# Kernel optimization log

Measured on AMD Instinct MI355X. Metric: run time of the kernel, lower is better.

Reference implementation:

```python
import math
import jax, jax.numpy as jnp
import numpy as np

B, N, D = 32, 1025, 768
K, CD, TD = 64, 128, 256  # num_clusters, cluster_dim, token_dim
REG = 0.1
NUM_ITERS = 5


def setup_inputs() -> dict:
    key = jax.random.key(0)
    ks = jax.random.split(key, 8)
    x = jax.random.normal(ks[0], (B, N, D), dtype=jnp.float32)
    # Linear params (torch nn.Linear: y = x @ W.T + b; we store W already transposed as [in, out])
    Wf = jax.random.normal(ks[1], (D, CD), dtype=jnp.float32) / math.sqrt(D)
    bf = jnp.zeros((CD,), dtype=jnp.float32)
    Ws = jax.random.normal(ks[2], (D, K), dtype=jnp.float32) / math.sqrt(D)
    bs = jnp.zeros((K,), dtype=jnp.float32)
    Wt = jax.random.normal(ks[3], (D, TD), dtype=jnp.float32) / math.sqrt(D)
    bt = jnp.zeros((TD,), dtype=jnp.float32)
    anchors = jax.random.normal(ks[4], (K, CD), dtype=jnp.float32) * 0.1
    dust_bin = jnp.float32(1.0)
    sharpness = jnp.float32(5.0)
    return {"x": x, "Wf": Wf, "bf": bf, "Ws": Ws, "bs": bs, "Wt": Wt, "bt": bt,
            "anchors": anchors, "dust_bin": dust_bin, "sharpness": sharpness}


def _log_otp_solver(log_a, log_b, M, num_iters, reg):
    M = M / reg
    u = jnp.zeros_like(log_a)  # [B, K+1]
    v = jnp.zeros_like(log_b)  # [B, N-1]
    for _ in range(num_iters):
        u = log_a - jax.nn.logsumexp(M + v[:, None, :], axis=2)
        v = log_b - jax.nn.logsumexp(M + u[:, :, None], axis=1)
    return M + u[:, :, None] + v[:, None, :]


def reference(x, Wf, bf, Ws, bs, Wt, bt, anchors, dust_bin, sharpness):
    b, n, d = x.shape
    t_global = x[:, 0]            # [B, D]
    fi = x[:, 1:]                 # [B, N-1, D]
    f = fi @ Wf + bf              # [B, N-1, CD]
    s = jnp.swapaxes(fi @ Ws + bs, 1, 2)  # [B, K, N-1]
    t = t_global @ Wt + bt        # [B, TD]
    s = s * sharpness
    dust = jnp.broadcast_to(dust_bin, (b, 1, n - 1))
    s_aug = jnp.concatenate([s, dust], axis=1)  # [B, K+1, N-1]
    log_a = jnp.full((b, K + 1), -math.log(K + 1), dtype=x.dtype)
    log_b = jnp.full((b, n - 1), -math.log(n - 1), dtype=x.dtype)
    log_P = _log_otp_solver(log_a, log_b, s_aug, NUM_ITERS, REG)
    p = jnp.exp(log_P)[:, :-1, :]  # [B, K, N-1]
    # v_agg = sum_n p[b,k,n] * (2*f[b,n,:] - anchors[k,:])  (algebraic rewrite of the broadcast sum)
    v_agg = 2.0 * jnp.einsum('bkn,bnc->bkc', p, f) - p.sum(axis=2)[:, :, None] * anchors[None]
    v_local = v_agg.reshape(b, -1)            # [B, K*CD]
    f_out = jnp.concatenate([t, v_local], axis=-1)
    norm = jnp.maximum(jnp.linalg.norm(f_out, axis=-1, keepdims=True), 1e-12)
    return f_out / norm
```

## Files before the change

### kernel.cpp

```cpp
#include <hip/hip_runtime.h>
#include <math.h>


#define BATCH 32
#define NTOK  1025
#define DIM   768
#define KDIM  64
#define CDIM  128
#define TDIM  256
#define NM1   1024
#define ROWLEN 8448
#define NITER 5
#define INV_REG 10.0f
#define NS_AGG 8
#define LOG_A (-4.17438727f)
#define LOG_B (-6.93147181f)

typedef __attribute__((ext_vector_type(8))) short short8;
typedef __attribute__((ext_vector_type(4))) float floatx4;

typedef __attribute__((address_space(3))) unsigned int lds_uint;
typedef const __attribute__((address_space(1))) unsigned int glb_uint;

__device__ __forceinline__ void gload_lds16(const void* g, void* l) {
    __builtin_amdgcn_global_load_lds((glb_uint*)g, (lds_uint*)l, 16, 0, 0);
}

__device__ __forceinline__ unsigned short bf16_rne(float f) {
    unsigned u = __builtin_bit_cast(unsigned, f);
    unsigned r = u + 0x7FFFu + ((u >> 16) & 1u);
    return (unsigned short)(r >> 16);
}

__device__ __forceinline__ short8 cvt8(float4 a, float4 b) {
    short8 r;
    r[0] = (short)bf16_rne(a.x); r[1] = (short)bf16_rne(a.y);
    r[2] = (short)bf16_rne(a.z); r[3] = (short)bf16_rne(a.w);
    r[4] = (short)bf16_rne(b.x); r[5] = (short)bf16_rne(b.y);
    r[6] = (short)bf16_rne(b.z); r[7] = (short)bf16_rne(b.w);
    return r;
}

__global__ __launch_bounds__(256) void prep(
    const float* __restrict__ Wf, const float* __restrict__ Ws,
    const float* __restrict__ bf, const float* __restrict__ bs,
    const float* __restrict__ x, const float* __restrict__ Wt,
    short* __restrict__ W_pack, float* __restrict__ bias_all,
    float* __restrict__ tpart)
{
    __shared__ float xr[256];
    const int blk = blockIdx.x, tid = threadIdx.x;
    if (blk < 576) {
        int idx = blk * 256 + tid;
        int g    = idx / 6144;
        int rem  = idx - g * 6144;
        int nf   = rem >> 9;
        int rem2 = rem & 511;
        int lane = rem2 >> 3;
        int j    = rem2 & 7;
        int k = g * 32 + (lane >> 4) * 8 + j;
        int c = nf * 16 + (lane & 15);
        float v = (c < CDIM) ? Wf[(size_t)k * CDIM + c] : Ws[(size_t)k * KDIM + (c - CDIM)];
        W_pack[idx] = (short)bf16_rne(v);
        if (idx < 192) bias_all[idx] = (idx < CDIM) ? bf[idx] : bs[idx - CDIM];
    } else {
        int i = blk - 576;
        int b = i / 3, dy = i - b * 3;
        xr[tid] = x[(size_t)b * NTOK * DIM + (size_t)dy * 256 + tid];
        __syncthreads();
        float acc = 0.f;
        const float* wp = Wt + (size_t)dy * 256 * TDIM + tid;
#pragma unroll 8
        for (int d = 0; d < 256; ++d) acc = fmaf(xr[d], wp[(size_t)d * TDIM], acc);
        tpart[((size_t)dy * BATCH + b) * TDIM + tid] = acc;
    }
}

__global__ __launch_bounds__(256, 2) void gemm_fs(
    const float* __restrict__ x, const short* __restrict__ W_pack,
    const float* __restrict__ bias_all, const float* __restrict__ sharp_p,
    const float* __restrict__ dust_p,
    unsigned short* __restrict__ fT, float* __restrict__ Mmat,
    float2* __restrict__ part0)
{
    __shared__ __align__(16) short Bs[12288];
    __shared__ __align__(16) short As[4096];
    __shared__ float2 sm[4][4][16];
    const int tid  = threadIdx.x;
    const int wave = tid >> 6, lane = tid & 63;
    const int quad = lane >> 4, lrow = lane & 15;
    const int bb0   = blockIdx.x & 31;
    const int chunk = blockIdx.x >> 5;
    const int R = bb0 * 1024 + chunk * 64 + wave * 16;

    const int arow = bb0 * 1024 + chunk * 64 + (tid >> 2);
    const float* asrc = x + ((size_t)(arow >> 10) * NTOK + 1 + (arow & 1023)) * DIM + (tid & 3) * 16;
    const int r    = (tid >> 2) & 15;
    const int seg  = tid & 3;
    const int kk_w = seg >> 1;
    const int q0   = (seg & 1) * 2;
    short* adst0 = &As[(((tid >> 6) * 2 + kk_w) * 64 + q0 * 16 + r) * 8];
    short* adst1 = &As[(((tid >> 6) * 2 + kk_w) * 64 + (q0 + 1) * 16 + r) * 8];

    floatx4 acc[12];
#pragma unroll
    for (int nf = 0; nf < 12; ++nf) acc[nf] = (floatx4){0.f, 0.f, 0.f, 0.f};

    float4 g0 = *(const float4*)(asrc);
    float4 g1 = *(const float4*)(asrc + 4);
    float4 g2 = *(const float4*)(asrc + 8);
    float4 g3 = *(const float4*)(asrc + 12);

    for (int ko = 0; ko < 12; ++ko) {
        __syncthreads();
        const short* bsrc = W_pack + ko * 12288 + tid * 8;
#pragma unroll
        for (int i = 0; i < 6; ++i)
            gload_lds16(bsrc + i * 2048, &Bs[i * 2048 + tid * 8]);
        *(short8*)adst0 = cvt8(g0, g1);
        *(short8*)adst1 = cvt8(g2, g3);
        __syncthreads();
        if (ko < 11) {
            const float* ap = asrc + (ko + 1) * 64;
            g0 = *(const float4*)(ap);
            g1 = *(const float4*)(ap + 4);
            g2 = *(const float4*)(ap + 8);
            g3 = *(const float4*)(ap + 12);
            __builtin_amdgcn_sched_barrier(0);
        }
#pragma unroll
        for (int kk = 0; kk < 2; ++kk) {
            short8 af = *(const short8*)&As[((wave * 2 + kk) * 64 + lane) * 8];
#pragma unroll
            for (int nf = 0; nf < 12; ++nf) {
                short8 bf8 = *(const short8*)&Bs[((kk * 12 + nf) * 64 + lane) * 8];
                acc[nf] = __builtin_amdgcn_mfma_f32_16x16x32_bf16(af, bf8, acc[nf], 0, 0, 0);
            }
        }
    }

    const float sc = sharp_p[0] * INV_REG;
    const float dustM = dust_p[0] * INV_REG;
    const int bb = R >> 10;
    const int tok = (R & 1023) + quad * 4;
#pragma unroll
    for (int nf = 0; nf < 12; ++nf) {
        const int c = nf * 16 + lrow;
        const float bias = bias_all[c];
        if (nf < 8) {
            ushort4 w;
            w.x = bf16_rne(acc[nf][0] + bias);
            w.y = bf16_rne(acc[nf][1] + bias);
            w.z = bf16_rne(acc[nf][2] + bias);
            w.w = bf16_rne(acc[nf][3] + bias);
            *(ushort4*)(fT + ((size_t)bb * CDIM + c) * NM1 + tok) = w;
        } else {
            const int k = c - CDIM;
            float4 w = make_float4((acc[nf][0] + bias) * sc, (acc[nf][1] + bias) * sc,
                                   (acc[nf][2] + bias) * sc, (acc[nf][3] + bias) * sc);
            *(float4*)(Mmat + ((size_t)bb * KDIM + k) * NM1 + tok) = w;
            float m = fmaxf(fmaxf(w.x, w.y), fmaxf(w.z, w.w));
            m = fmaxf(m, __shfl_xor(m, 16));
            m = fmaxf(m, __shfl_xor(m, 32));
            float e = __expf(w.x - m) + __expf(w.y - m)
                    + __expf(w.z - m) + __expf(w.w - m);
            e += __shfl_xor(e, 16);
            e += __shfl_xor(e, 32);
            if (quad == 0) sm[wave][nf - 8][lrow] = make_float2(m, e);
        }
    }
    __syncthreads();
    if (tid < 65) {
        float2 o;
        if (tid < 64) {
            float2 p0 = sm[0][tid >> 4][tid & 15];
            float2 p1 = sm[1][tid >> 4][tid & 15];
            float2 p2 = sm[2][tid >> 4][tid & 15];
            float2 p3 = sm[3][tid >> 4][tid & 15];
            float m = fmaxf(fmaxf(p0.x, p1.x), fmaxf(p2.x, p3.x));
            float e = p0.y * __expf(p0.x - m) + p1.y * __expf(p1.x - m)
                    + p2.y * __expf(p2.x - m) + p3.y * __expf(p3.x - m);
            o = make_float2(m, e);
        } else {
            o = make_float2(dustM, 64.f);
        }
        part0[((size_t)bb0 * 16 + chunk) * 65 + tid] = o;
    }
}

__global__ __launch_bounds__(256) void sink_u(
    const float* __restrict__ Mmat, const float* __restrict__ v_in,
    const float* __restrict__ dust_p, float* __restrict__ u_out)
{
    const int b   = blockIdx.x & 31;
    const int sub = blockIdx.x >> 5;
    const int k   = sub * 4 + (threadIdx.x >> 6);
    if (k > 64) return;
    const int lane = threadIdx.x & 63;
    const float dustM = dust_p[0] * INV_REG;

    const float4* vp = (const float4*)(v_in + (size_t)b * NM1);
    float xs[16];
    if (k < 64) {
        const float4* Mp = (const float4*)(Mmat + ((size_t)b * KDIM + k) * NM1);
#pragma unroll
        for (int i = 0; i < 4; ++i) {
            float4 mv = Mp[i * 64 + lane];
            float4 vv = vp[i * 64 + lane];
            xs[i * 4 + 0] = mv.x + vv.x;
            xs[i * 4 + 1] = mv.y + vv.y;
            xs[i * 4 + 2] = mv.z + vv.z;
            xs[i * 4 + 3] = mv.w + vv.w;
        }
    } else {
#pragma unroll
        for (int i = 0; i < 4; ++i) {
            float4 vv = vp[i * 64 + lane];
            xs[i * 4 + 0] = dustM + vv.x;
            xs[i * 4 + 1] = dustM + vv.y;
            xs[i * 4 + 2] = dustM + vv.z;
            xs[i * 4 + 3] = dustM + vv.w;
        }
    }
    float m = xs[0];
#pragma unroll
    for (int i = 1; i < 16; ++i) m = fmaxf(m, xs[i]);
#pragma unroll
    for (int off = 1; off < 64; off <<= 1) m = fmaxf(m, __shfl_xor(m, off));
    float S = 0.f;
#pragma unroll
    for (int i = 0; i < 16; ++i) S += __expf(xs[i] - m);
#pragma unroll
    for (int off = 1; off < 64; off <<= 1) S += __shfl_xor(S, off);
    if (lane == 0) u_out[b * 65 + k] = LOG_A - (m + __logf(S));
}

template<bool UPART>
__global__ __launch_bounds__(256) void sink_v(
    const float* __restrict__ Mmat, const float* __restrict__ u_in,
    const float2* __restrict__ part0,
    const float* __restrict__ dust_p, float* __restrict__ v_out)
{
    __shared__ float us[65];
    __shared__ float2 pp[4][64];
    const int b   = blockIdx.x & 31;
    const int ns2 = blockIdx.x >> 5;
    const int tid = threadIdx.x;
    const int tok = tid & 63, kq = tid >> 6;
    const int n = ns2 * 64 + tok;
    if (tid < 65) {
        if (UPART) {
            const float2* pr = part0 + (size_t)b * 16 * 65 + tid;
            float M2 = -3.4e38f;
            float2 pv[16];
#pragma unroll
            for (int q = 0; q < 16; ++q) { pv[q] = pr[q * 65]; M2 = fmaxf(M2, pv[q].x); }
            float S2 = 0.f;
#pragma unroll
            for (int q = 0; q < 16; ++q) S2 += pv[q].y * __expf(pv[q].x - M2);
            us[tid] = LOG_A - (M2 + __logf(S2));
        } else {
            us[tid] = u_in[b * 65 + tid];
        }
    }
    __syncthreads();
    const float* Mb = Mmat + ((size_t)b * KDIM + kq * 16) * NM1 + n;
    float xs[16];
#pragma unroll
    for (int kk = 0; kk < 16; ++kk) xs[kk] = Mb[(size_t)kk * NM1] + us[kq * 16 + kk];
    float m = xs[0];
#pragma unroll
    for (int kk = 1; kk < 16; ++kk) m = fmaxf(m, xs[kk]);
    float e = 0.f;
#pragma unroll
    for (int kk = 0; kk < 16; ++kk) e += __expf(xs[kk] - m);
    pp[kq][tok] = make_float2(m, e);
    __syncthreads();
    if (tid < 64) {
        const float xd = dust_p[0] * INV_REG + us[64];
        float m3 = xd;
#pragma unroll
        for (int q = 0; q < 4; ++q) m3 = fmaxf(m3, pp[q][tid].x);
        float S3 = __expf(xd - m3);
#pragma unroll
        for (int q = 0; q < 4; ++q) S3 += pp[q][tid].y * __expf(pp[q][tid].x - m3);
        v_out[(size_t)b * NM1 + ns2 * 64 + tid] = LOG_B - (m3 + __logf(S3));
    }
}

__global__ __launch_bounds__(256) void aggregate(
    const float* __restrict__ Mmat, const unsigned short* __restrict__ fT,
    const float* __restrict__ u_in, const float* __restrict__ dust_p,
    float* __restrict__ vpart, float* __restrict__ rspart)
{
    __shared__ float us[65];
    __shared__ __align__(16) float vsh[128];
    __shared__ float wv[4][128][2];
    const int b = blockIdx.x, ns = blockIdx.y;
    const int tid = threadIdx.x;
    const int wave = tid >> 6, lane = tid & 63;
    const int quad = lane >> 4, lrow = lane & 15;
    const int krow = wave * 16 + lrow;
    const float dustM = dust_p[0] * INV_REG;

    if (tid < 65) us[tid] = u_in[b * 65 + tid];
    __syncthreads();

    float mreg[32];
    {
        const float* Mrow = Mmat + ((size_t)b * KDIM + krow) * NM1 + ns * 128 + quad * 8;
#pragma unroll
        for (int s = 0; s < 4; ++s) {
            float4 a = *(const float4*)(Mrow + s * 32);
            float4 c = *(const float4*)(Mrow + s * 32 + 4);
            mreg[s*8+0]=a.x; mreg[s*8+1]=a.y; mreg[s*8+2]=a.z; mreg[s*8+3]=a.w;
            mreg[s*8+4]=c.x; mreg[s*8+5]=c.y; mreg[s*8+6]=c.z; mreg[s*8+7]=c.w;
        }
    }

    const float uk = us[krow];
#pragma unroll
    for (int s = 0; s < 4; ++s) {
#pragma unroll
        for (int j = 0; j < 8; ++j) {
            float x = mreg[s*8+j] + uk;
            float m2 = x;
            m2 = fmaxf(m2, __shfl_xor(m2, 1));
            m2 = fmaxf(m2, __shfl_xor(m2, 2));
            m2 = fmaxf(m2, __shfl_xor(m2, 4));
            m2 = fmaxf(m2, __shfl_xor(m2, 8));
            float e = __expf(x - m2);
            e += __shfl_xor(e, 1);
            e += __shfl_xor(e, 2);
            e += __shfl_xor(e, 4);
            e += __shfl_xor(e, 8);
            if (lrow == 0) {
                wv[wave][s*32 + quad*8 + j][0] = m2;
                wv[wave][s*32 + quad*8 + j][1] = e;
            }
        }
    }
    __syncthreads();
    if (tid < 128) {
        const float xd = dustM + us[64];
        float m3 = xd;
#pragma unroll
        for (int w = 0; w < 4; ++w) m3 = fmaxf(m3, wv[w][tid][0]);
        float S3 = __expf(xd - m3);
#pragma unroll
        for (int w = 0; w < 4; ++w) S3 += wv[w][tid][1] * __expf(wv[w][tid][0] - m3);
        vsh[tid] = LOG_B - (m3 + __logf(S3));
    }
    __syncthreads();

    const unsigned short* fbase = fT + ((size_t)b * CDIM + lrow) * NM1 + ns * 128 + quad * 8;
    floatx4 acc[8];
#pragma unroll
    for (int nf = 0; nf < 8; ++nf) acc[nf] = (floatx4){0.f, 0.f, 0.f, 0.f};
    float rs = 0.f;
#pragma unroll
    for (int s = 0; s < 4; ++s) {
        const int tb = s * 32 + quad * 8;
        float4 v0 = *(const float4*)&vsh[tb];
        float4 v1 = *(const float4*)&vsh[tb + 4];
        float p[8];
        p[0] = __expf(mreg[s*8+0] + uk + v0.x);
        p[1] = __expf(mreg[s*8+1] + uk + v0.y);
        p[2] = __expf(mreg[s*8+2] + uk + v0.z);
        p[3] = __expf(mreg[s*8+3] + uk + v0.w);
        p[4] = __expf(mreg[s*8+4] + uk + v1.x);
        p[5] = __expf(mreg[s*8+5] + uk + v1.y);
        p[6] = __expf(mreg[s*8+6] + uk + v1.z);
        p[7] = __expf(mreg[s*8+7] + uk + v1.w);
        short8 afrag;
#pragma unroll
        for (int j = 0; j < 8; ++j) {
            rs += p[j];
            afrag[j] = (short)bf16_rne(p[j]);
        }
#pragma unroll
        for (int nf = 0; nf < 8; ++nf) {
            short8 bfrag = *(const short8*)(fbase + (size_t)nf * 16 * NM1 + s * 32);
            acc[nf] = __builtin_amdgcn_mfma_f32_16x16x32_bf16(afrag, bfrag, acc[nf], 0, 0, 0);
        }
    }
    rs += __shfl_xor(rs, 16);
    rs += __shfl_xor(rs, 32);
    if (lane < 16) rspart[(ns * BATCH + b) * KDIM + krow] = rs;

    float* vp = vpart + (size_t)(ns * BATCH + b) * (KDIM * CDIM);
#pragma unroll
    for (int nf = 0; nf < 8; ++nf) {
        const int c = nf * 16 + lrow;
#pragma unroll
        for (int j = 0; j < 4; ++j)
            vp[(size_t)(wave * 16 + quad * 4 + j) * CDIM + c] = acc[nf][j];
    }
}

__global__ __launch_bounds__(1024) void finalize_all(
    const float* __restrict__ vpart, const float* __restrict__ rspart,
    const float* __restrict__ anchors, const float* __restrict__ tpart,
    const float* __restrict__ bt, float* __restrict__ out)
{
    __shared__ float rstot[KDIM];
    __shared__ float red[16];
    __shared__ float sc_sh;
    const int b = blockIdx.x, tid = threadIdx.x;
    const int lane = tid & 63, wave = tid >> 6;

    if (tid < KDIM) {
        float s = 0.f;
#pragma unroll
        for (int ns = 0; ns < NS_AGG; ++ns)
            s += rspart[(ns * BATCH + b) * KDIM + tid];
        rstot[tid] = s;
    }
    __syncthreads();

    const size_t e0 = (size_t)tid * 8;
    float4 s0 = make_float4(0.f, 0.f, 0.f, 0.f);
    float4 s1 = make_float4(0.f, 0.f, 0.f, 0.f);
#pragma unroll
    for (int ns = 0; ns < NS_AGG; ++ns) {
        const float* vp = vpart + (size_t)(ns * BATCH + b) * (KDIM * CDIM) + e0;
        float4 a = *(const float4*)(vp);
        float4 c = *(const float4*)(vp + 4);
        s0.x += a.x; s0.y += a.y; s0.z += a.z; s0.w += a.w;
        s1.x += c.x; s1.y += c.y; s1.z += c.z; s1.w += c.w;
    }
    const float rsv = rstot[tid >> 4];
    float4 a0 = *(const float4*)(anchors + e0);
    float4 a1 = *(const float4*)(anchors + e0 + 4);
    float4 v0, v1;
    v0.x = 2.f * s0.x - rsv * a0.x;  v0.y = 2.f * s0.y - rsv * a0.y;
    v0.z = 2.f * s0.z - rsv * a0.z;  v0.w = 2.f * s0.w - rsv * a0.w;
    v1.x = 2.f * s1.x - rsv * a1.x;  v1.y = 2.f * s1.y - rsv * a1.y;
    v1.z = 2.f * s1.z - rsv * a1.z;  v1.w = 2.f * s1.w - rsv * a1.w;
    float ss = v0.x*v0.x + v0.y*v0.y + v0.z*v0.z + v0.w*v0.w
             + v1.x*v1.x + v1.y*v1.y + v1.z*v1.z + v1.w*v1.w;

    float t = 0.f;
    if (tid < TDIM) {
        t = bt[tid];
#pragma unroll
        for (int s = 0; s < 3; ++s) t += tpart[((size_t)s * BATCH + b) * TDIM + tid];
        ss += t * t;
    }

#pragma unroll
    for (int off = 32; off > 0; off >>= 1) ss += __shfl_down(ss, off);
    if (lane == 0) red[wave] = ss;
    __syncthreads();
    if (tid == 0) {
        float tot = 0.f;
#pragma unroll
        for (int i = 0; i < 16; ++i) tot += red[i];
        sc_sh = 1.f / fmaxf(sqrtf(tot), 1e-12f);
    }
    __syncthreads();
    const float scale = sc_sh;

    float* orow = out + (size_t)b * ROWLEN;
    if (tid < TDIM) orow[tid] = t * scale;
    v0.x *= scale; v0.y *= scale; v0.z *= scale; v0.w *= scale;
    v1.x *= scale; v1.y *= scale; v1.z *= scale; v1.w *= scale;
    *(float4*)&orow[TDIM + e0]     = v0;
    *(float4*)&orow[TDIM + e0 + 4] = v1;
}

extern "C" void kernel_launch(void* const* d_in, const int* in_sizes, int n_in,
                              void* d_out, int out_size, void* d_ws, size_t ws_size,
                              hipStream_t stream)
{
    const float* x       = (const float*)d_in[0];
    const float* Wf      = (const float*)d_in[1];
    const float* bf      = (const float*)d_in[2];
    const float* Ws      = (const float*)d_in[3];
    const float* bs      = (const float*)d_in[4];
    const float* Wt      = (const float*)d_in[5];
    const float* bt      = (const float*)d_in[6];
    const float* anchors = (const float*)d_in[7];
    const float* dust    = (const float*)d_in[8];
    const float* sharp   = (const float*)d_in[9];
    float* out = (float*)d_out;

    char* base = (char*)d_ws;
    short* W_pack        = (short*)base;
    float* bias_all      = (float*)(base + 294912);
    float* Mmat          = bias_all + 192;
    unsigned short* fT   = (unsigned short*)(Mmat + (size_t)BATCH * KDIM * NM1);
    float* u_buf         = (float*)(fT + (size_t)BATCH * CDIM * NM1);
    float* v_buf         = u_buf + BATCH * 65;
    float2* part0        = (float2*)(v_buf + BATCH * NM1);
    float* vpart         = (float*)(part0 + (size_t)BATCH * 16 * 65);
    float* rspart        = vpart + (size_t)NS_AGG * BATCH * KDIM * CDIM;
    float* tpart         = rspart + NS_AGG * BATCH * KDIM;

    hipLaunchKernelGGL(prep, dim3(672), dim3(256), 0, stream,
                       Wf, Ws, bf, bs, x, Wt, W_pack, bias_all, tpart);
    hipLaunchKernelGGL(gemm_fs, dim3(512), dim3(256), 0, stream,
                       x, W_pack, bias_all, sharp, dust, fT, Mmat, part0);

    hipLaunchKernelGGL(HIP_KERNEL_NAME(sink_v<true>), dim3(512), dim3(256), 0, stream,
                       Mmat, u_buf, part0, dust, v_buf);
    for (int it = 1; it < NITER; ++it) {
        hipLaunchKernelGGL(sink_u, dim3(544), dim3(256), 0, stream,
                           Mmat, v_buf, dust, u_buf);
        if (it < NITER - 1)
            hipLaunchKernelGGL(HIP_KERNEL_NAME(sink_v<false>), dim3(512), dim3(256), 0, stream,
                               Mmat, u_buf, part0, dust, v_buf);
    }

    hipLaunchKernelGGL(aggregate, dim3(BATCH, NS_AGG), dim3(256), 0, stream,
                       Mmat, fT, u_buf, dust, vpart, rspart);
    hipLaunchKernelGGL(finalize_all, dim3(BATCH), dim3(1024), 0, stream,
                       vpart, rspart, anchors, tpart, bt, out);
}
```

Before: 238.6 us.

## Fuse Sinkhorn u and v updates into one kernel using partial logsumexp

```diff
diff --git a/kernel.cpp b/kernel.cpp
--- a/kernel.cpp
+++ b/kernel.cpp
@@ -188,109 +188,95 @@
     }
 }
 
-__global__ __launch_bounds__(256) void sink_u(
-    const float* __restrict__ Mmat, const float* __restrict__ v_in,
-    const float* __restrict__ dust_p, float* __restrict__ u_out)
-{
-    const int b   = blockIdx.x & 31;
-    const int sub = blockIdx.x >> 5;
-    const int k   = sub * 4 + (threadIdx.x >> 6);
-    if (k > 64) return;
-    const int lane = threadIdx.x & 63;
-    const float dustM = dust_p[0] * INV_REG;
-
-    const float4* vp = (const float4*)(v_in + (size_t)b * NM1);
-    float xs[16];
-    if (k < 64) {
-        const float4* Mp = (const float4*)(Mmat + ((size_t)b * KDIM + k) * NM1);
-#pragma unroll
-        for (int i = 0; i < 4; ++i) {
-            float4 mv = Mp[i * 64 + lane];
-            float4 vv = vp[i * 64 + lane];
-            xs[i * 4 + 0] = mv.x + vv.x;
-            xs[i * 4 + 1] = mv.y + vv.y;
-            xs[i * 4 + 2] = mv.z + vv.z;
-            xs[i * 4 + 3] = mv.w + vv.w;
-        }
-    } else {
-#pragma unroll
-        for (int i = 0; i < 4; ++i) {
-            float4 vv = vp[i * 64 + lane];
-            xs[i * 4 + 0] = dustM + vv.x;
-            xs[i * 4 + 1] = dustM + vv.y;
-            xs[i * 4 + 2] = dustM + vv.z;
-            xs[i * 4 + 3] = dustM + vv.w;
-        }
-    }
-    float m = xs[0];
-#pragma unroll
-    for (int i = 1; i < 16; ++i) m = fmaxf(m, xs[i]);
-#pragma unroll
-    for (int off = 1; off < 64; off <<= 1) m = fmaxf(m, __shfl_xor(m, off));
-    float S = 0.f;
-#pragma unroll
-    for (int i = 0; i < 16; ++i) S += __expf(xs[i] - m);
-#pragma unroll
-    for (int off = 1; off < 64; off <<= 1) S += __shfl_xor(S, off);
-    if (lane == 0) u_out[b * 65 + k] = LOG_A - (m + __logf(S));
-}
-
-template<bool UPART>
-__global__ __launch_bounds__(256) void sink_v(
-    const float* __restrict__ Mmat, const float* __restrict__ u_in,
-    const float2* __restrict__ part0,
-    const float* __restrict__ dust_p, float* __restrict__ v_out)
+__global__ __launch_bounds__(256) void sink_vu(
+    const float* __restrict__ Mmat, const float* __restrict__ dust_p,
+    const float2* __restrict__ pin, float2* __restrict__ pout)
 {
     __shared__ float us[65];
     __shared__ float2 pp[4][64];
+    __shared__ float vsh[64];
+    __shared__ float yb[64][65];
     const int b   = blockIdx.x & 31;
     const int ns2 = blockIdx.x >> 5;
     const int tid = threadIdx.x;
     const int tok = tid & 63, kq = tid >> 6;
     const int n = ns2 * 64 + tok;
+    const float dustM = dust_p[0] * INV_REG;
+
+    float mreg[16];
+    const float* Mb = Mmat + ((size_t)b * KDIM + kq * 16) * NM1 + n;
+#pragma unroll
+    for (int kk = 0; kk < 16; ++kk) mreg[kk] = Mb[(size_t)kk * NM1];
+
     if (tid < 65) {
-        if (UPART) {
-            const float2* pr = part0 + (size_t)b * 16 * 65 + tid;
-            float M2 = -3.4e38f;
-            float2 pv[16];
-#pragma unroll
-            for (int q = 0; q < 16; ++q) { pv[q] = pr[q * 65]; M2 = fmaxf(M2, pv[q].x); }
-            float S2 = 0.f;
-#pragma unroll
-            for (int q = 0; q < 16; ++q) S2 += pv[q].y * __expf(pv[q].x - M2);
-            us[tid] = LOG_A - (M2 + __logf(S2));
-        } else {
-            us[tid] = u_in[b * 65 + tid];
-        }
-    }
-    __syncthreads();
-    const float* Mb = Mmat + ((size_t)b * KDIM + kq * 16) * NM1 + n;
-    float xs[16];
-#pragma unroll
-    for (int kk = 0; kk < 16; ++kk) xs[kk] = Mb[(size_t)kk * NM1] + us[kq * 16 + kk];
-    float m = xs[0];
-#pragma unroll
-    for (int kk = 1; kk < 16; ++kk) m = fmaxf(m, xs[kk]);
-    float e = 0.f;
-#pragma unroll
-    for (int kk = 0; kk < 16; ++kk) e += __expf(xs[kk] - m);
-    pp[kq][tok] = make_float2(m, e);
+        const float2* pr = pin + (size_t)b * 16 * 65 + tid;
+        float M2 = -3.4e38f;
+        float2 pv[16];
+#pragma unroll
+        for (int q = 0; q < 16; ++q) { pv[q] = pr[q * 65]; M2 = fmaxf(M2, pv[q].x); }
+        float S2 = 0.f;
+#pragma unroll
+        for (int q = 0; q < 16; ++q) S2 += pv[q].y * __expf(pv[q].x - M2);
+        us[tid] = LOG_A - (M2 + __logf(S2));
+    }
+    __syncthreads();
+
+    {
+        float m = mreg[0] + us[kq * 16];
+#pragma unroll
+        for (int kk = 1; kk < 16; ++kk) m = fmaxf(m, mreg[kk] + us[kq * 16 + kk]);
+        float e = 0.f;
+#pragma unroll
+        for (int kk = 0; kk < 16; ++kk) e += __expf(mreg[kk] + us[kq * 16 + kk] - m);
+        pp[kq][tok] = make_float2(m, e);
+    }
     __syncthreads();
     if (tid < 64) {
-        const float xd = dust_p[0] * INV_REG + us[64];
+        const float xd = dustM + us[64];
         float m3 = xd;
 #pragma unroll
         for (int q = 0; q < 4; ++q) m3 = fmaxf(m3, pp[q][tid].x);
         float S3 = __expf(xd - m3);
 #pragma unroll
         for (int q = 0; q < 4; ++q) S3 += pp[q][tid].y * __expf(pp[q][tid].x - m3);
-        v_out[(size_t)b * NM1 + ns2 * 64 + tid] = LOG_B - (m3 + __logf(S3));
+        vsh[tid] = LOG_B - (m3 + __logf(S3));
+    }
+    __syncthreads();
+
+    const float v = vsh[tok];
+#pragma unroll
+    for (int kk = 0; kk < 16; ++kk) yb[kq * 16 + kk][tok] = mreg[kk] + v;
+    if (kq == 0) {
+        float mv = v;
+#pragma unroll
+        for (int off = 1; off < 64; off <<= 1) mv = fmaxf(mv, __shfl_xor(mv, off));
+        float ev = __expf(v - mv);
+#pragma unroll
+        for (int off = 1; off < 64; off <<= 1) ev += __shfl_xor(ev, off);
+        if (tok == 0) pout[((size_t)b * 16 + ns2) * 65 + 64] = make_float2(dustM + mv, ev);
+    }
+    __syncthreads();
+    {
+        const int rr = tid >> 2, tq = tid & 3;
+        float mm = yb[rr][tq * 16];
+#pragma unroll
+        for (int i = 1; i < 16; ++i) mm = fmaxf(mm, yb[rr][tq * 16 + i]);
+        float ee = 0.f;
+#pragma unroll
+        for (int i = 0; i < 16; ++i) ee += __expf(yb[rr][tq * 16 + i] - mm);
+        float m1 = __shfl_xor(mm, 1), e1 = __shfl_xor(ee, 1);
+        float mo = fmaxf(mm, m1);
+        ee = ee * __expf(mm - mo) + e1 * __expf(m1 - mo); mm = mo;
+        float m2 = __shfl_xor(mm, 2), e2 = __shfl_xor(ee, 2);
+        mo = fmaxf(mm, m2);
+        ee = ee * __expf(mm - mo) + e2 * __expf(m2 - mo); mm = mo;
+        if (tq == 0) pout[((size_t)b * 16 + ns2) * 65 + rr] = make_float2(mm, ee);
     }
 }
 
 __global__ __launch_bounds__(256) void aggregate(
     const float* __restrict__ Mmat, const unsigned short* __restrict__ fT,
-    const float* __restrict__ u_in, const float* __restrict__ dust_p,
+    const float2* __restrict__ pin, const float* __restrict__ dust_p,
     float* __restrict__ vpart, float* __restrict__ rspart)
 {
     __shared__ float us[65];
@@ -303,7 +289,17 @@
     const int krow = wave * 16 + lrow;
     const float dustM = dust_p[0] * INV_REG;
 
-    if (tid < 65) us[tid] = u_in[b * 65 + tid];
+    if (tid < 65) {
+        const float2* pr = pin + (size_t)b * 16 * 65 + tid;
+        float M2 = -3.4e38f;
+        float2 pv[16];
+#pragma unroll
+        for (int q = 0; q < 16; ++q) { pv[q] = pr[q * 65]; M2 = fmaxf(M2, pv[q].x); }
+        float S2 = 0.f;
+#pragma unroll
+        for (int q = 0; q < 16; ++q) S2 += pv[q].y * __expf(pv[q].x - M2);
+        us[tid] = LOG_A - (M2 + __logf(S2));
+    }
     __syncthreads();
 
     float mreg[32];
@@ -490,10 +486,9 @@
     float* bias_all      = (float*)(base + 294912);
     float* Mmat          = bias_all + 192;
     unsigned short* fT   = (unsigned short*)(Mmat + (size_t)BATCH * KDIM * NM1);
-    float* u_buf         = (float*)(fT + (size_t)BATCH * CDIM * NM1);
-    float* v_buf         = u_buf + BATCH * 65;
-    float2* part0        = (float2*)(v_buf + BATCH * NM1);
-    float* vpart         = (float*)(part0 + (size_t)BATCH * 16 * 65);
+    float2* part0        = (float2*)(fT + (size_t)BATCH * CDIM * NM1);
+    float2* part1        = part0 + (size_t)BATCH * 16 * 65;
+    float* vpart         = (float*)(part1 + (size_t)BATCH * 16 * 65);
     float* rspart        = vpart + (size_t)NS_AGG * BATCH * KDIM * CDIM;
     float* tpart         = rspart + NS_AGG * BATCH * KDIM;
 
@@ -502,18 +497,17 @@
     hipLaunchKernelGGL(gemm_fs, dim3(512), dim3(256), 0, stream,
                        x, W_pack, bias_all, sharp, dust, fT, Mmat, part0);
 
-    hipLaunchKernelGGL(HIP_KERNEL_NAME(sink_v<true>), dim3(512), dim3(256), 0, stream,
-                       Mmat, u_buf, part0, dust, v_buf);
-    for (int it = 1; it < NITER; ++it) {
-        hipLaunchKernelGGL(sink_u, dim3(544), dim3(256), 0, stream,
-                           Mmat, v_buf, dust, u_buf);
-        if (it < NITER - 1)
-            hipLaunchKernelGGL(HIP_KERNEL_NAME(sink_v<false>), dim3(512), dim3(256), 0, stream,
-                               Mmat, u_buf, part0, dust, v_buf);
-    }
+    hipLaunchKernelGGL(sink_vu, dim3(512), dim3(256), 0, stream,
+                       Mmat, dust, part0, part1);
+    hipLaunchKernelGGL(sink_vu, dim3(512), dim3(256), 0, stream,
+                       Mmat, dust, part1, part0);
+    hipLaunchKernelGGL(sink_vu, dim3(512), dim3(256), 0, stream,
+                       Mmat, dust, part0, part1);
+    hipLaunchKernelGGL(sink_vu, dim3(512), dim3(256), 0, stream,
+                       Mmat, dust, part1, part0);
 
     hipLaunchKernelGGL(aggregate, dim3(BATCH, NS_AGG), dim3(256), 0, stream,
-                       Mmat, fT, u_buf, dust, vpart, rspart);
+                       Mmat, fT, part0, dust, vpart, rspart);
     hipLaunchKernelGGL(finalize_all, dim3(BATCH), dim3(1024), 0, stream,
                        vpart, rspart, anchors, tpart, bt, out);
 }
```

After: 232.2 us. -2.7%, faster.
